# Kernel tuning notes

Measured on AMD Instinct MI355X. Metric: run time of the kernel, lower is better.

## Reference

```python
import jax, jax.numpy as jnp
import numpy as np

M_A, N_B, S_A, S_B = 2, 2, 1, 1  # sharing chunks and base strides


def setup_inputs() -> dict:
    key = jax.random.key(0)
    ks = jax.random.split(key, 7)
    B, S, D_IN, D_OUT = 4, 2048, 4096, 4096
    U, SHARED_R = 8, 56  # rank=64, unshared u=8
    x = jax.random.normal(ks[0], (B, S, D_IN), jnp.float32)
    W = jax.random.normal(ks[1], (D_OUT, D_IN), jnp.float32) * 0.02
    b = jax.random.normal(ks[2], (D_OUT,), jnp.float32) * 0.02
    A_u = jax.random.normal(ks[3], (U, D_IN), jnp.float32) * 0.02
    B_u = jax.random.normal(ks[4], (D_OUT, U), jnp.float32) * 0.02
    A0_shared = jax.random.normal(ks[5], (SHARED_R, D_IN // M_A), jnp.float32) * 0.02
    B0_shared = jax.random.normal(ks[6], (D_OUT // N_B, SHARED_R), jnp.float32) * 0.02
    return {"x": x, "W": W, "b": b, "A_u": A_u, "B_u": B_u,
            "A0_shared": A0_shared, "B0_shared": B0_shared}


def reference(x, W, b, A_u, B_u, A0_shared, B0_shared):
    # Rotated shared chunks: roll A0 along rank dim (axis 0), tile along in dim.
    A_s = jnp.concatenate([jnp.roll(A0_shared, i * S_A, axis=0) for i in range(M_A)], axis=1)  # [r_s, in]
    # Roll B0 along rank dim (axis 1), tile along out dim.
    B_s = jnp.concatenate([jnp.roll(B0_shared, i * S_B, axis=1) for i in range(N_B)], axis=0)  # [out, r_s]
    # Full delta_W materialization, as in the original module.
    delta_W = B_u @ A_u + B_s @ A_s  # [out, in]
    original = jnp.einsum('bsd,od->bso', x, W) + b
    adapt = jnp.einsum('bsd,od->bso', x, delta_W)
    return original + adapt
```

## Files before the change

### kernel.cpp

```cpp
#include <hip/hip_runtime.h>

typedef unsigned short u16;
typedef __bf16 bf16x8 __attribute__((ext_vector_type(8)));
typedef float f32x4 __attribute__((ext_vector_type(4)));
typedef u16 u16x8 __attribute__((ext_vector_type(8)));

#define M_DIM 8192
#define N_DIM 4096
#define K_DIM 4096
#define BM 256
#define BN 256
#define BK 64
#define NT (K_DIM / BK)

__device__ __forceinline__ u16 f2b(float f) {
  unsigned int x = __float_as_uint(f);
  unsigned int r = (x + 0x7fffu + ((x >> 16) & 1u)) >> 16;
  return (u16)r;
}

#define GLOAD_LDS16(gp, lp)                                        \
  __builtin_amdgcn_global_load_lds(                                \
      (const __attribute__((address_space(1))) void*)(gp),         \
      (__attribute__((address_space(3))) void*)(lp), 16, 0, 0)

#define SB0 __builtin_amdgcn_sched_barrier(0)
#define BAR                                                        \
  do {                                                             \
    SB0;                                                           \
    __builtin_amdgcn_s_barrier();                                  \
    SB0;                                                           \
  } while (0)
#define VMW(N)                                                     \
  do {                                                             \
    SB0;                                                           \
    asm volatile("s_waitcnt vmcnt(" #N ")" ::: "memory");          \
    SB0;                                                           \
  } while (0)

__global__ __launch_bounds__(256) void cvt_x(const float* __restrict__ X,
                                             u16* __restrict__ Xb) {
  const size_t t = (size_t)blockIdx.x * 256 + threadIdx.x;
  const f32x4* src = (const f32x4*)X + t * 2;
  f32x4 a = src[0];
  f32x4 b = src[1];
  u16x8 o;
  o[0] = f2b(a[0]); o[1] = f2b(a[1]); o[2] = f2b(a[2]); o[3] = f2b(a[3]);
  o[4] = f2b(b[0]); o[5] = f2b(b[1]); o[6] = f2b(b[2]); o[7] = f2b(b[3]);
  *((u16x8*)Xb + t) = o;
}

__global__ __launch_bounds__(256) void build_weff(
    const float* __restrict__ W, const float* __restrict__ Au,
    const float* __restrict__ Bu, const float* __restrict__ A0,
    const float* __restrict__ B0, u16* __restrict__ Weff) {
  __shared__ float coef[64 * 16];
  const int t = threadIdx.x;
  const int o0 = blockIdx.y * 16;

#pragma unroll
  for (int j = 0; j < 4; j++) {
    const int idx = t + j * 256;
    const int r = idx >> 4;
    const int oi = idx & 15;
    const int o = o0 + oi;
    float v;
    if (r < 8) {
      v = Bu[o * 8 + r];
    } else {
      const int rs = r - 8;
      if (o < 2048) {
        v = B0[o * 56 + rs];
      } else {
        const int rr = rs ? (rs - 1) : 55;
        v = B0[(o - 2048) * 56 + rr];
      }
    }
    coef[r * 16 + oi] = v;
  }
  __syncthreads();

  const int d0 = blockIdx.x * 1024 + t * 4;
  const int hi = (d0 >= 2048);
  const int dd = hi ? (d0 - 2048) : d0;

  f32x4 acc[16] = {};

#pragma unroll
  for (int r = 0; r < 8; r++) {
    f32x4 a = *(const f32x4*)(Au + (size_t)r * 4096 + d0);
    const float* cr = &coef[r * 16];
#pragma unroll
    for (int oi = 0; oi < 16; oi++) {
      const float c = cr[oi];
      acc[oi][0] += c * a[0]; acc[oi][1] += c * a[1];
      acc[oi][2] += c * a[2]; acc[oi][3] += c * a[3];
    }
  }
#pragma unroll 4
  for (int rs = 0; rs < 56; rs++) {
    const int rr = hi ? (rs ? (rs - 1) : 55) : rs;
    f32x4 a = *(const f32x4*)(A0 + (size_t)rr * 2048 + dd);
    const float* cr = &coef[(rs + 8) * 16];
#pragma unroll
    for (int oi = 0; oi < 16; oi++) {
      const float c = cr[oi];
      acc[oi][0] += c * a[0]; acc[oi][1] += c * a[1];
      acc[oi][2] += c * a[2]; acc[oi][3] += c * a[3];
    }
  }

#pragma unroll
  for (int oi = 0; oi < 16; oi++) {
    f32x4 w = *(const f32x4*)(W + (size_t)(o0 + oi) * 4096 + d0);
    ushort4 ov;
    ov.x = f2b(acc[oi][0] + w[0]);
    ov.y = f2b(acc[oi][1] + w[1]);
    ov.z = f2b(acc[oi][2] + w[2]);
    ov.w = f2b(acc[oi][3] + w[3]);
    *(ushort4*)(Weff + (size_t)(o0 + oi) * 4096 + d0) = ov;
  }
}

__global__ __launch_bounds__(512, 2) void gemm_bt_bias(
    const u16* __restrict__ X, const u16* __restrict__ Wf,
    const float* __restrict__ bias, float* __restrict__ C) {
  __shared__ __align__(16) u16 lds[65536];

  const int tid = threadIdx.x;
  const int wave = tid >> 6;
  const int lane = tid & 63;
  const int wm = wave >> 2;
  const int wn = wave & 3;
  const int quad = lane >> 4;
  const int l16 = lane & 15;

  const int wgid = ((blockIdx.x & 7) << 6) | (blockIdx.x >> 3);
  const int n0 = (wgid & 15) * BN;
  const int m0 = (wgid >> 4) * BM;

  const int srow = lane >> 3;
  const int sq = lane & 7;
  const int scol = ((sq ^ srow) << 3);
  const u16* xg = X + (size_t)(m0 + wave * 8 + srow) * K_DIM + scol;
  const u16* wg = Wf + (size_t)(n0 + wave * 8 + srow) * K_DIM + scol;
  u16* lA = lds + wave * 512;
  u16* lB = lds + 32768 + wave * 512;

#define SG_A(b, r, t)                                                       \
  GLOAD_LDS16(xg + (size_t)(r) * 64 * K_DIM + (size_t)(t) * BK,             \
              lA + (b) * 16384 + (r) * 4096)
#define SG_B(b, r, t)                                                       \
  GLOAD_LDS16(wg + (size_t)(r) * 64 * K_DIM + (size_t)(t) * BK,             \
              lB + (b) * 16384 + (r) * 4096)

  f32x4 acc[8][4] = {};
  bf16x8 afr[4][2];
  bf16x8 bfr[2][2][2];

  const int c0 = (quad << 4) ^ ((l16 & 7) << 4);

#define READ_A(mh)                                                          \
  do {                                                                      \
    const char* ab_ = Ab + (size_t)((wm * 128 + (mh) * 64 + l16) * 128);    \
    _Pragma("unroll") for (int mi = 0; mi < 4; mi++) {                      \
      afr[mi][0] = *(const bf16x8*)(ab_ + mi * 2048 + c0);                  \
      afr[mi][1] = *(const bf16x8*)(ab_ + mi * 2048 + (c0 ^ 64));           \
    }                                                                       \
  } while (0)

#define READ_B(nh)                                                          \
  do {                                                                      \
    const char* bb_ = Bb + (size_t)((wn * 64 + (nh) * 32 + l16) * 128);     \
    _Pragma("unroll") for (int ni = 0; ni < 2; ni++) {                      \
      bfr[nh][ni][0] = *(const bf16x8*)(bb_ + ni * 2048 + c0);              \
      bfr[nh][ni][1] = *(const bf16x8*)(bb_ + ni * 2048 + (c0 ^ 64));       \
    }                                                                       \
  } while (0)

#define MFMA_Q(mh, nh)                                                      \
  do {                                                                      \
    __builtin_amdgcn_s_setprio(1);                                          \
    _Pragma("unroll") for (int mi = 0; mi < 4; mi++) {                      \
      _Pragma("unroll") for (int ni = 0; ni < 2; ni++) {                    \
        acc[(mh)*4 + mi][(nh)*2 + ni] =                                     \
            __builtin_amdgcn_mfma_f32_16x16x32_bf16(                        \
                afr[mi][0], bfr[nh][ni][0],                                 \
                acc[(mh)*4 + mi][(nh)*2 + ni], 0, 0, 0);                    \
        acc[(mh)*4 + mi][(nh)*2 + ni] =                                     \
            __builtin_amdgcn_mfma_f32_16x16x32_bf16(                        \
                afr[mi][1], bfr[nh][ni][1],                                 \
                acc[(mh)*4 + mi][(nh)*2 + ni], 0, 0, 0);                    \
      }                                                                     \
    }                                                                       \
    __builtin_amdgcn_s_setprio(0);                                          \
  } while (0)

  SG_A(0, 0, 0); SG_A(0, 2, 0);
  SG_B(0, 0, 0); SG_B(0, 1, 0);
  SG_B(0, 2, 0); SG_B(0, 3, 0);
  SG_A(0, 1, 0); SG_A(0, 3, 0);
  SG_A(1, 0, 1); SG_A(1, 2, 1);
  VMW(4);
  BAR;

  for (int t = 0; t < NT; ++t) {
    const int buf = t & 1;
    const char* Ab = (const char*)lds + buf * 32768;
    const char* Bb = (const char*)lds + 65536 + buf * 32768;
    const int t1 = (t + 1 < NT) ? t + 1 : NT - 1;
    const int t2 = (t + 2 < NT) ? t + 2 : NT - 1;
    const int b1 = (t + 1) & 1;
    const int b2 = buf;

    READ_A(0);
    READ_B(0);
    SG_B(b1, 0, t1); SG_B(b1, 1, t1);
    BAR;
    MFMA_Q(0, 0);
    BAR;

    READ_B(1);
    SG_B(b1, 2, t1); SG_B(b1, 3, t1);
    BAR;
    MFMA_Q(0, 1);
    VMW(6);
    BAR;

    READ_A(1);
    SG_A(b1, 1, t1); SG_A(b1, 3, t1);
    BAR;
    MFMA_Q(1, 1);
    BAR;

    SG_A(b2, 0, t2); SG_A(b2, 2, t2);
    BAR;
    MFMA_Q(1, 0);
    VMW(4);
    BAR;
  }
  VMW(0);

#pragma unroll
  for (int j = 0; j < 4; j++) {
    const int col = n0 + wn * 64 + j * 16 + l16;
    const float bv = bias[col];
#pragma unroll
    for (int i = 0; i < 8; i++) {
      const int row = m0 + wm * 128 + i * 16 + quad * 4;
#pragma unroll
      for (int r = 0; r < 4; r++) {
        C[(size_t)(row + r) * N_DIM + col] = acc[i][j][r] + bv;
      }
    }
  }
}

extern "C" void kernel_launch(void* const* d_in, const int* in_sizes, int n_in,
                              void* d_out, int out_size, void* d_ws, size_t ws_size,
                              hipStream_t stream) {
  const float* x  = (const float*)d_in[0];
  const float* W  = (const float*)d_in[1];
  const float* b  = (const float*)d_in[2];
  const float* Au = (const float*)d_in[3];
  const float* Bu = (const float*)d_in[4];
  const float* A0 = (const float*)d_in[5];
  const float* B0 = (const float*)d_in[6];
  float* out = (float*)d_out;

  u16* Xb   = (u16*)d_ws;
  u16* Weff = (u16*)((char*)d_ws + (size_t)64 * 1024 * 1024);

  cvt_x<<<16384, 256, 0, stream>>>(x, Xb);
  build_weff<<<dim3(4, 256), 256, 0, stream>>>(W, Au, Bu, A0, B0, Weff);
  gemm_bt_bias<<<dim3(512), dim3(512), 0, stream>>>(Xb, Weff, b, out);
}
```

Baseline: 551.9 us.

## Prefetch next-tile LDS fragments across iterations and relax scheduling barriers

Moves the READ_A(0)/READ_B(0)/READ_B(1) LDS fragment loads for the next K tile to the end of the previous iteration, with a prologue before the loop, so they overlap with the loop tail. READ_A(1) is moved to sit after the MFMA_Q(0,1) quadrant. The sched_barrier fences around s_barrier are removed, giving the compiler more freedom to interleave LDS reads with MFMAs. This risks LDS hazards: B fragments for buffer b1 are read while later SG_B writes still target that buffer, and the waitcnt placement has changed, so correctness depends on the barrier ordering.

Result: no change. 551.0 us (-0.2%).

```diff
diff --git a/kernel.cpp b/kernel.cpp
--- a/kernel.cpp
+++ b/kernel.cpp
@@ -24,18 +24,11 @@
       (const __attribute__((address_space(1))) void*)(gp),         \
       (__attribute__((address_space(3))) void*)(lp), 16, 0, 0)
 
-#define SB0 __builtin_amdgcn_sched_barrier(0)
-#define BAR                                                        \
-  do {                                                             \
-    SB0;                                                           \
-    __builtin_amdgcn_s_barrier();                                  \
-    SB0;                                                           \
-  } while (0)
+#define BAR __builtin_amdgcn_s_barrier()
 #define VMW(N)                                                     \
   do {                                                             \
-    SB0;                                                           \
     asm volatile("s_waitcnt vmcnt(" #N ")" ::: "memory");          \
-    SB0;                                                           \
+    __builtin_amdgcn_sched_barrier(0);                             \
   } while (0)
 
 __global__ __launch_bounds__(256) void cvt_x(const float* __restrict__ X,
@@ -160,18 +153,20 @@
 
   const int c0 = (quad << 4) ^ ((l16 & 7) << 4);
 
-#define READ_A(mh)                                                          \
+#define READ_A(mh, ABASE)                                                   \
   do {                                                                      \
-    const char* ab_ = Ab + (size_t)((wm * 128 + (mh) * 64 + l16) * 128);    \
+    const char* ab_ =                                                       \
+        (ABASE) + (size_t)((wm * 128 + (mh) * 64 + l16) * 128);             \
     _Pragma("unroll") for (int mi = 0; mi < 4; mi++) {                      \
       afr[mi][0] = *(const bf16x8*)(ab_ + mi * 2048 + c0);                  \
       afr[mi][1] = *(const bf16x8*)(ab_ + mi * 2048 + (c0 ^ 64));           \
     }                                                                       \
   } while (0)
 
-#define READ_B(nh)                                                          \
+#define READ_B(nh, BBASE)                                                   \
   do {                                                                      \
-    const char* bb_ = Bb + (size_t)((wn * 64 + (nh) * 32 + l16) * 128);     \
+    const char* bb_ =                                                       \
+        (BBASE) + (size_t)((wn * 64 + (nh) * 32 + l16) * 128);              \
     _Pragma("unroll") for (int ni = 0; ni < 2; ni++) {                      \
       bfr[nh][ni][0] = *(const bf16x8*)(bb_ + ni * 2048 + c0);              \
       bfr[nh][ni][1] = *(const bf16x8*)(bb_ + ni * 2048 + (c0 ^ 64));       \
@@ -203,31 +198,34 @@
   SG_A(1, 0, 1); SG_A(1, 2, 1);
   VMW(4);
   BAR;
+  {
+    const char* Ab0 = (const char*)lds;
+    const char* Bb0 = (const char*)lds + 65536;
+    READ_A(0, Ab0);
+    READ_B(0, Bb0);
+    READ_B(1, Bb0);
+  }
 
   for (int t = 0; t < NT; ++t) {
     const int buf = t & 1;
     const char* Ab = (const char*)lds + buf * 32768;
-    const char* Bb = (const char*)lds + 65536 + buf * 32768;
     const int t1 = (t + 1 < NT) ? t + 1 : NT - 1;
     const int t2 = (t + 2 < NT) ? t + 2 : NT - 1;
     const int b1 = (t + 1) & 1;
     const int b2 = buf;
 
-    READ_A(0);
-    READ_B(0);
     SG_B(b1, 0, t1); SG_B(b1, 1, t1);
     BAR;
     MFMA_Q(0, 0);
-    BAR;
-
-    READ_B(1);
+    VMW(4);
+    BAR;
+
     SG_B(b1, 2, t1); SG_B(b1, 3, t1);
     BAR;
     MFMA_Q(0, 1);
-    VMW(6);
-    BAR;
-
-    READ_A(1);
+    READ_A(1, Ab);
+    BAR;
+
     SG_A(b1, 1, t1); SG_A(b1, 3, t1);
     BAR;
     MFMA_Q(1, 1);
@@ -238,6 +236,13 @@
     MFMA_Q(1, 0);
     VMW(4);
     BAR;
+    {
+      const char* AbN = (const char*)lds + b1 * 32768;
+      const char* BbN = (const char*)lds + 65536 + b1 * 32768;
+      READ_A(0, AbN);
+      READ_B(0, BbN);
+      READ_B(1, BbN);
+    }
   }
   VMW(0);
 
```
